# Kernel tuning notes

Hardware: AMD Instinct MI355X
Metric: run time of the kernel (lower is better)

The kernel has to match this reference:

```python
import jax, jax.numpy as jnp
import numpy as np

N_NODES = 50000
N_EDGES = 640000
D = 128
L = 3
LN_EPS = 1e-5


def _layer_norm(x, g, b):
    mu = jnp.mean(x, axis=-1, keepdims=True)
    var = jnp.mean(jnp.square(x - mu), axis=-1, keepdims=True)
    return (x - mu) * jax.lax.rsqrt(var + LN_EPS) * g + b


def setup_inputs() -> dict:
    key = jax.random.key(0)
    ks = jax.random.split(key, 8)
    scale = 1.0 / np.sqrt(D)
    x = jax.random.normal(ks[0], (N_NODES, D), dtype=jnp.float32)
    edge_index = jax.random.randint(ks[1], (2, N_EDGES), 0, N_NODES, dtype=jnp.int32)
    return {
        "x": x,
        "edge_index": edge_index,
        "eps": jnp.zeros((L,), jnp.float32),  # GIN epsilon, init 0.0
        "W1": jax.random.normal(ks[2], (L, D, D), jnp.float32) * scale,
        "b1": jnp.zeros((L, D), jnp.float32),
        "W2": jax.random.normal(ks[3], (L, D, D), jnp.float32) * scale,
        "b2": jnp.zeros((L, D), jnp.float32),
        "ln_g": jnp.ones((L, D), jnp.float32),   # per-conv LayerNorm
        "ln_b": jnp.zeros((L, D), jnp.float32),
        "skip_g": jnp.ones((L - 1, D), jnp.float32),  # outer norms for layers 0..L-2
        "skip_b": jnp.zeros((L - 1, D), jnp.float32),
    }


def reference(x, edge_index, eps, W1, b1, W2, b2, ln_g, ln_b, skip_g, skip_b):
    src = edge_index[0]
    dst = edge_index[1]
    h = x  # no input_norm (use_input_norm=False)
    for i in range(L):
        h_in = h
        # scatter-add neighbor aggregation: out[dst] += h[src]
        agg = jax.ops.segment_sum(h[src], dst, num_segments=N_NODES)
        z = (1.0 + eps[i]) * h + agg
        # 2-layer MLP: Linear -> ReLU -> Linear
        z = jnp.maximum(z @ W1[i] + b1[i], 0.0) @ W2[i] + b2[i]
        z = _layer_norm(z, ln_g[i], ln_b[i])
        if i < L - 1:
            z = _layer_norm(z, skip_g[i], skip_b[i])  # skip-path norm
            z = jnp.maximum(z, 0.0)  # ReLU; dropout is identity in eval
        h = z + h_in  # residual (shapes always match: in==hidden)
    return h
```

## Files before the change

### kernel.cpp

```cpp
#include <hip/hip_runtime.h>
#include <hip/hip_bf16.h>

#define N_NODES 50000
#define N_EDGES 640000
#define D 128
#define NPAD 50048
#define LAYERS 3
#define SCAN_NB 196

typedef __attribute__((ext_vector_type(4))) float f32x4;
typedef __attribute__((ext_vector_type(8))) short bf16x8;
typedef __attribute__((ext_vector_type(4))) short bf16x4;

static __device__ __forceinline__ short f2bf(float f) {
    union { float f; unsigned u; } x; x.f = f;
    unsigned r = x.u + 0x7fffu + ((x.u >> 16) & 1u);
    return (short)(r >> 16);
}
static __device__ __forceinline__ float bf2f(short s) {
    union { unsigned u; float f; } x; x.u = ((unsigned)(unsigned short)s) << 16;
    return x.f;
}

__global__ void init_kernel(const f32x4* __restrict__ in, bf16x4* __restrict__ hb) {
    int t = blockIdx.x * 256 + threadIdx.x;
    f32x4 v = in[t];
    bf16x4 p; p[0] = f2bf(v.x); p[1] = f2bf(v.y); p[2] = f2bf(v.z); p[3] = f2bf(v.w);
    hb[t] = p;
}

__global__ void prepw_kernel(const float* __restrict__ W1, const float* __restrict__ W2,
                             short* __restrict__ wt) {
    int t = blockIdx.x * 256 + threadIdx.x;
    if (t >= 6 * 16384) return;
    int m = t >> 14, rem = t & 16383;
    int c = rem >> 7, k = rem & 127;
    const float* src = (m < 3) ? (W1 + m * 16384) : (W2 + (m - 3) * 16384);
    wt[m * 16384 + c * 128 + k] = f2bf(src[k * 128 + c]);
}

__global__ void hist_kernel(const int* __restrict__ dst, int* __restrict__ deg) {
    int e = blockIdx.x * 256 + threadIdx.x;
    if (e < N_EDGES) atomicAdd(&deg[dst[e]], 1);
}

__global__ void scan1_kernel(const int* __restrict__ deg, int* __restrict__ rs,
                             int* __restrict__ bsum) {
    __shared__ int tmp[256];
    int i = blockIdx.x * 256 + threadIdx.x;
    int v = (i < N_NODES) ? deg[i] : 0;
    tmp[threadIdx.x] = v;
    __syncthreads();
    for (int off = 1; off < 256; off <<= 1) {
        int t = (threadIdx.x >= off) ? tmp[threadIdx.x - off] : 0;
        __syncthreads();
        tmp[threadIdx.x] += t;
        __syncthreads();
    }
    if (i < N_NODES) rs[i] = tmp[threadIdx.x] - v;
    if (threadIdx.x == 255) bsum[blockIdx.x] = tmp[255];
}

__global__ void scan2_kernel(int* __restrict__ bsum) {
    __shared__ int tmp[256];
    int v = (threadIdx.x < SCAN_NB) ? bsum[threadIdx.x] : 0;
    tmp[threadIdx.x] = v;
    __syncthreads();
    for (int off = 1; off < 256; off <<= 1) {
        int t = (threadIdx.x >= off) ? tmp[threadIdx.x - off] : 0;
        __syncthreads();
        tmp[threadIdx.x] += t;
        __syncthreads();
    }
    if (threadIdx.x < SCAN_NB) bsum[threadIdx.x] = tmp[threadIdx.x] - v;
}

__global__ void scan3_kernel(int* __restrict__ rs, const int* __restrict__ bsum) {
    int i = blockIdx.x * 256 + threadIdx.x;
    if (i < N_NODES) rs[i] += bsum[blockIdx.x];
}

__global__ void fill_kernel(const int* __restrict__ src, const int* __restrict__ dst,
                            const int* __restrict__ rs, int* __restrict__ cursor,
                            int* __restrict__ col) {
    int e = blockIdx.x * 256 + threadIdx.x;
    if (e >= N_EDGES) return;
    int d = dst[e];
    int p = atomicAdd(&cursor[d], 1);
    col[rs[d] + p] = src[e];
}

__global__ __launch_bounds__(256) void agg_kernel(const bf16x8* __restrict__ hb,
                                                  const int* __restrict__ rs,
                                                  const int* __restrict__ deg,
                                                  const int* __restrict__ col,
                                                  const float* __restrict__ epsArr, int layer,
                                                  bf16x8* __restrict__ z) {
    int t = blockIdx.x * 256 + threadIdx.x;
    int node = t >> 4, lane = t & 15;
    if (node >= NPAD) return;
    bf16x8 o;
    if (node < N_NODES) {
        float acc[8] = {0.f, 0.f, 0.f, 0.f, 0.f, 0.f, 0.f, 0.f};
        int start = rs[node], dg = deg[node];
        const int* cp = col + start;
        for (int base = 0; base < dg; base += 16) {
            int n = dg - base; n = n < 16 ? n : 16;
            int my = (lane < n) ? cp[base + lane] : 0;
            bf16x8 v[16];
#pragma unroll
            for (int j = 0; j < 16; ++j) {
                if (j < n) {
                    int idx = __shfl(my, j, 16);
                    v[j] = hb[(size_t)idx * 16 + lane];
                }
            }
#pragma unroll
            for (int j = 0; j < 16; ++j) {
                if (j < n) {
#pragma unroll
                    for (int e = 0; e < 8; ++e) acc[e] += bf2f(v[j][e]);
                }
            }
        }
        float s = 1.0f + epsArr[layer];
        bf16x8 hv = hb[(size_t)node * 16 + lane];
#pragma unroll
        for (int e = 0; e < 8; ++e) o[e] = f2bf(fmaf(s, bf2f(hv[e]), acc[e]));
    } else {
        o = (bf16x8)(short)0;
    }
    z[(size_t)node * 16 + lane] = o;
}

template <bool LAST>
__global__ __launch_bounds__(256, 2) void mlp_kernel(const short* __restrict__ Z,
                                                     const short* __restrict__ Wt1,
                                                     const float* __restrict__ B1,
                                                     const short* __restrict__ Wt2,
                                                     const float* __restrict__ B2,
                                                     const float* __restrict__ G1,
                                                     const float* __restrict__ Bt1,
                                                     const float* __restrict__ G2,
                                                     const float* __restrict__ Bt2,
                                                     const float* __restrict__ RS,
                                                     float* __restrict__ H,
                                                     short* __restrict__ HB) {
    __shared__ __align__(16) char lds[49152 + 3072];
    const int t = threadIdx.x;
    const int wave = t >> 6, lane = t & 63;
    const int r = lane & 15, kq = lane >> 4;
    const int lrow = wave * 16 + r;
    const int row = blockIdx.x * 64 + lrow;
    const int swzr = (r & 7) << 4;
    const int swzl = (lrow & 7) << 4;
    const int fcol = kq * 16;

    const short* Zr = Z + (size_t)row * D + kq * 8;
    bf16x8 zb0 = *(const bf16x8*)(Zr);
    bf16x8 zb1 = *(const bf16x8*)(Zr + 32);
    bf16x8 zb2 = *(const bf16x8*)(Zr + 64);
    bf16x8 zb3 = *(const bf16x8*)(Zr + 96);
    __builtin_amdgcn_sched_barrier(0);

    bf16x8 g2[8];
    {
        bf16x8 g1[8];
#pragma unroll
        for (int i = 0; i < 8; ++i) g1[i] = *(const bf16x8*)(Wt1 + i * 2048 + t * 8);
#pragma unroll
        for (int i = 0; i < 8; ++i) g2[i] = *(const bf16x8*)(Wt2 + i * 2048 + t * 8);
        if (t < (LAST ? 128 : 192)) {
            int which = t >> 5, chunk = t & 31;
            const float* vp = (which == 0) ? B1 : (which == 1) ? B2 : (which == 2) ? G1
                            : (which == 3) ? Bt1 : (which == 4) ? G2 : Bt2;
            *(f32x4*)(lds + 49152 + which * 512 + chunk * 16) = *(const f32x4*)(vp + chunk * 4);
        }
#pragma unroll
        for (int i = 0; i < 8; ++i) {
            int b = i * 4096 + t * 16;
            *(bf16x8*)(lds + (b ^ (((b >> 8) & 7) << 4))) = g1[i];
        }
    }
    __syncthreads();

    bf16x4 p[8];
#pragma unroll
    for (int ct = 0; ct < 8; ++ct) {
        int wb = (ct * 16 + r) * 256 + kq * 16;
        f32x4 acc = {0.f, 0.f, 0.f, 0.f};
        acc = __builtin_amdgcn_mfma_f32_16x16x32_bf16(*(const bf16x8*)(lds + ((wb      ) ^ swzr)), zb0, acc, 0, 0, 0);
        acc = __builtin_amdgcn_mfma_f32_16x16x32_bf16(*(const bf16x8*)(lds + ((wb +  64) ^ swzr)), zb1, acc, 0, 0, 0);
        acc = __builtin_amdgcn_mfma_f32_16x16x32_bf16(*(const bf16x8*)(lds + ((wb + 128) ^ swzr)), zb2, acc, 0, 0, 0);
        acc = __builtin_amdgcn_mfma_f32_16x16x32_bf16(*(const bf16x8*)(lds + ((wb + 192) ^ swzr)), zb3, acc, 0, 0, 0);
        f32x4 bias = *(const f32x4*)(lds + 49152 + 0 + ct * 64 + fcol);
        p[ct][0] = f2bf(fmaxf(acc[0] + bias.x, 0.0f));
        p[ct][1] = f2bf(fmaxf(acc[1] + bias.y, 0.0f));
        p[ct][2] = f2bf(fmaxf(acc[2] + bias.z, 0.0f));
        p[ct][3] = f2bf(fmaxf(acc[3] + bias.w, 0.0f));
    }
    __syncthreads();

    f32x4 rsv[8] = {};
    if (row < N_NODES) {
#pragma unroll
        for (int ct = 0; ct < 8; ++ct)
            rsv[ct] = *(const f32x4*)(RS + (size_t)row * D + ct * 16 + kq * 4);
    }
    __builtin_amdgcn_sched_barrier(0);

#pragma unroll
    for (int i = 0; i < 8; ++i) {
        int b = i * 4096 + t * 16;
        *(bf16x8*)(lds + (b ^ (((b >> 8) & 7) << 4))) = g2[i];
    }
#pragma unroll
    for (int ct = 0; ct < 8; ++ct)
        *(bf16x4*)(lds + 32768 + ((lrow * 256 + ct * 32 + kq * 8) ^ swzl)) = p[ct];
    __syncthreads();

    bf16x8 hb0 = *(const bf16x8*)(lds + 32768 + ((lrow * 256 +   0 + kq * 16) ^ swzl));
    bf16x8 hb1 = *(const bf16x8*)(lds + 32768 + ((lrow * 256 +  64 + kq * 16) ^ swzl));
    bf16x8 hb2 = *(const bf16x8*)(lds + 32768 + ((lrow * 256 + 128 + kq * 16) ^ swzl));
    bf16x8 hb3 = *(const bf16x8*)(lds + 32768 + ((lrow * 256 + 192 + kq * 16) ^ swzl));

    f32x4 o[8];
#pragma unroll
    for (int ct = 0; ct < 8; ++ct) {
        int wb = (ct * 16 + r) * 256 + kq * 16;
        f32x4 acc = {0.f, 0.f, 0.f, 0.f};
        acc = __builtin_amdgcn_mfma_f32_16x16x32_bf16(*(const bf16x8*)(lds + ((wb      ) ^ swzr)), hb0, acc, 0, 0, 0);
        acc = __builtin_amdgcn_mfma_f32_16x16x32_bf16(*(const bf16x8*)(lds + ((wb +  64) ^ swzr)), hb1, acc, 0, 0, 0);
        acc = __builtin_amdgcn_mfma_f32_16x16x32_bf16(*(const bf16x8*)(lds + ((wb + 128) ^ swzr)), hb2, acc, 0, 0, 0);
        acc = __builtin_amdgcn_mfma_f32_16x16x32_bf16(*(const bf16x8*)(lds + ((wb + 192) ^ swzr)), hb3, acc, 0, 0, 0);
        f32x4 bias = *(const f32x4*)(lds + 49152 + 512 + ct * 64 + fcol);
        o[ct] = acc + bias;
    }

    float s = 0.f, q = 0.f;
#pragma unroll
    for (int ct = 0; ct < 8; ++ct) {
        s += o[ct].x + o[ct].y + o[ct].z + o[ct].w;
        q += o[ct].x * o[ct].x + o[ct].y * o[ct].y + o[ct].z * o[ct].z + o[ct].w * o[ct].w;
    }
    s += __shfl_xor(s, 16, 64); q += __shfl_xor(q, 16, 64);
    s += __shfl_xor(s, 32, 64); q += __shfl_xor(q, 32, 64);
    float mu = s * (1.0f / D);
    float rstd = rsqrtf(q * (1.0f / D) - mu * mu + 1e-5f);
#pragma unroll
    for (int ct = 0; ct < 8; ++ct) {
        f32x4 g = *(const f32x4*)(lds + 49152 + 1024 + ct * 64 + fcol);
        f32x4 b = *(const f32x4*)(lds + 49152 + 1536 + ct * 64 + fcol);
        o[ct] = (o[ct] - mu) * rstd * g + b;
    }

    if (!LAST) {
        float s2 = 0.f, q2 = 0.f;
#pragma unroll
        for (int ct = 0; ct < 8; ++ct) {
            s2 += o[ct].x + o[ct].y + o[ct].z + o[ct].w;
            q2 += o[ct].x * o[ct].x + o[ct].y * o[ct].y + o[ct].z * o[ct].z + o[ct].w * o[ct].w;
        }
        s2 += __shfl_xor(s2, 16, 64); q2 += __shfl_xor(q2, 16, 64);
        s2 += __shfl_xor(s2, 32, 64); q2 += __shfl_xor(q2, 32, 64);
        float mu2 = s2 * (1.0f / D);
        float rstd2 = rsqrtf(q2 * (1.0f / D) - mu2 * mu2 + 1e-5f);
#pragma unroll
        for (int ct = 0; ct < 8; ++ct) {
            f32x4 g = *(const f32x4*)(lds + 49152 + 2048 + ct * 64 + fcol);
            f32x4 b = *(const f32x4*)(lds + 49152 + 2560 + ct * 64 + fcol);
            f32x4 y = (o[ct] - mu2) * rstd2 * g + b;
            y.x = fmaxf(y.x, 0.f); y.y = fmaxf(y.y, 0.f);
            y.z = fmaxf(y.z, 0.f); y.w = fmaxf(y.w, 0.f);
            o[ct] = y;
        }
    }

    if (row < N_NODES) {
#pragma unroll
        for (int ct = 0; ct < 8; ++ct) {
            size_t off = (size_t)row * D + ct * 16 + kq * 4;
            f32x4 hv = rsv[ct] + o[ct];
            *(f32x4*)(H + off) = hv;
            if (!LAST) {
                bf16x4 pb;
                pb[0] = f2bf(hv.x); pb[1] = f2bf(hv.y); pb[2] = f2bf(hv.z); pb[3] = f2bf(hv.w);
                *(bf16x4*)(HB + off) = pb;
            }
        }
    }
}

extern "C" void kernel_launch(void* const* d_in, const int* in_sizes, int n_in,
                              void* d_out, int out_size, void* d_ws, size_t ws_size,
                              hipStream_t stream) {
    const float* x   = (const float*)d_in[0];
    const int*   ei  = (const int*)d_in[1];
    const float* eps = (const float*)d_in[2];
    const float* W1  = (const float*)d_in[3];
    const float* b1  = (const float*)d_in[4];
    const float* W2  = (const float*)d_in[5];
    const float* b2  = (const float*)d_in[6];
    const float* lng = (const float*)d_in[7];
    const float* lnb = (const float*)d_in[8];
    const float* skg = (const float*)d_in[9];
    const float* skb = (const float*)d_in[10];
    float* h = (float*)d_out;

    char* ws = (char*)d_ws;
    short* zbuf = (short*)ws;
    short* hbb  = (short*)(ws + 12812288);
    short* wt   = (short*)(ws + 25624576);
    int*   rs   = (int*)  (ws + 25821184);
    int*   deg  = (int*)  (ws + 26021376);
    int*   cur  = (int*)  (ws + 26221568);
    int*   col  = (int*)  (ws + 26421760);
    int*   bsum = (int*)  (ws + 28981760);

    const int* srcIdx = ei;
    const int* dstIdx = ei + N_EDGES;

    init_kernel<<<(N_NODES * 32) / 256, 256, 0, stream>>>((const f32x4*)x, (bf16x4*)hbb);
    prepw_kernel<<<(6 * 16384) / 256, 256, 0, stream>>>(W1, W2, wt);

    hipMemsetAsync(deg, 0, 2 * 200192, stream);
    hist_kernel<<<(N_EDGES + 255) / 256, 256, 0, stream>>>(dstIdx, deg);
    scan1_kernel<<<SCAN_NB, 256, 0, stream>>>(deg, rs, bsum);
    scan2_kernel<<<1, 256, 0, stream>>>(bsum);
    scan3_kernel<<<SCAN_NB, 256, 0, stream>>>(rs, bsum);
    fill_kernel<<<(N_EDGES + 255) / 256, 256, 0, stream>>>(srcIdx, dstIdx, rs, cur, col);

    for (int l = 0; l < LAYERS; ++l) {
        agg_kernel<<<NPAD / 16, 256, 0, stream>>>(
            (const bf16x8*)hbb, rs, deg, col, eps, l, (bf16x8*)zbuf);
        const float* rsrc = (l == 0) ? x : h;
        if (l < LAYERS - 1) {
            mlp_kernel<false><<<NPAD / 64, 256, 0, stream>>>(
                zbuf, wt + l * 16384, b1 + l * D, wt + (3 + l) * 16384, b2 + l * D,
                lng + l * D, lnb + l * D, skg + l * D, skb + l * D, rsrc, h, hbb);
        } else {
            mlp_kernel<true><<<NPAD / 64, 256, 0, stream>>>(
                zbuf, wt + l * 16384, b1 + l * D, wt + (3 + l) * 16384, b2 + l * D,
                lng + l * D, lnb + l * D, nullptr, nullptr, rsrc, h, nullptr);
        }
    }
}
```

Measured before the change: 251.9 us.

## Fuse neighbor aggregation into MLP kernel with ping-pong bf16 feature buffers

Merges the separate gather/aggregation kernel into the MLP kernel. Each block now gathers neighbor rows for its 64 nodes with 4 threads per node and stages the aggregated z tile in LDS, instead of writing z to global memory and reading it back. The bf16 node features are double-buffered across layers so a layer reads one buffer while writing the other. This removes one launch per layer and the z round-trip through global memory. The cost is a gather with less parallelism: 4 lanes per node, each issuing 64-byte loads, versus the old 16 lanes with a shuffle-based index broadcast. It also puts more register pressure on a kernel launched with 2 blocks per SM.

Measured after the change: 235.7 us. -6.4%, faster.

```diff
diff --git a/kernel.cpp b/kernel.cpp
--- a/kernel.cpp
+++ b/kernel.cpp
@@ -90,62 +90,23 @@
     col[rs[d] + p] = src[e];
 }
 
-__global__ __launch_bounds__(256) void agg_kernel(const bf16x8* __restrict__ hb,
-                                                  const int* __restrict__ rs,
-                                                  const int* __restrict__ deg,
-                                                  const int* __restrict__ col,
-                                                  const float* __restrict__ epsArr, int layer,
-                                                  bf16x8* __restrict__ z) {
-    int t = blockIdx.x * 256 + threadIdx.x;
-    int node = t >> 4, lane = t & 15;
-    if (node >= NPAD) return;
-    bf16x8 o;
-    if (node < N_NODES) {
-        float acc[8] = {0.f, 0.f, 0.f, 0.f, 0.f, 0.f, 0.f, 0.f};
-        int start = rs[node], dg = deg[node];
-        const int* cp = col + start;
-        for (int base = 0; base < dg; base += 16) {
-            int n = dg - base; n = n < 16 ? n : 16;
-            int my = (lane < n) ? cp[base + lane] : 0;
-            bf16x8 v[16];
-#pragma unroll
-            for (int j = 0; j < 16; ++j) {
-                if (j < n) {
-                    int idx = __shfl(my, j, 16);
-                    v[j] = hb[(size_t)idx * 16 + lane];
-                }
-            }
-#pragma unroll
-            for (int j = 0; j < 16; ++j) {
-                if (j < n) {
-#pragma unroll
-                    for (int e = 0; e < 8; ++e) acc[e] += bf2f(v[j][e]);
-                }
-            }
-        }
-        float s = 1.0f + epsArr[layer];
-        bf16x8 hv = hb[(size_t)node * 16 + lane];
-#pragma unroll
-        for (int e = 0; e < 8; ++e) o[e] = f2bf(fmaf(s, bf2f(hv[e]), acc[e]));
-    } else {
-        o = (bf16x8)(short)0;
-    }
-    z[(size_t)node * 16 + lane] = o;
-}
-
 template <bool LAST>
-__global__ __launch_bounds__(256, 2) void mlp_kernel(const short* __restrict__ Z,
-                                                     const short* __restrict__ Wt1,
-                                                     const float* __restrict__ B1,
-                                                     const short* __restrict__ Wt2,
-                                                     const float* __restrict__ B2,
-                                                     const float* __restrict__ G1,
-                                                     const float* __restrict__ Bt1,
-                                                     const float* __restrict__ G2,
-                                                     const float* __restrict__ Bt2,
-                                                     const float* __restrict__ RS,
-                                                     float* __restrict__ H,
-                                                     short* __restrict__ HB) {
+__global__ __launch_bounds__(256, 2) void fused_kernel(const short* __restrict__ HBin,
+                                                       const int* __restrict__ rs,
+                                                       const int* __restrict__ deg,
+                                                       const int* __restrict__ col,
+                                                       const float* __restrict__ epsArr, int layer,
+                                                       const short* __restrict__ Wt1,
+                                                       const float* __restrict__ B1,
+                                                       const short* __restrict__ Wt2,
+                                                       const float* __restrict__ B2,
+                                                       const float* __restrict__ G1,
+                                                       const float* __restrict__ Bt1,
+                                                       const float* __restrict__ G2,
+                                                       const float* __restrict__ Bt2,
+                                                       const float* __restrict__ RS,
+                                                       float* __restrict__ H,
+                                                       short* __restrict__ HBout) {
     __shared__ __align__(16) char lds[49152 + 3072];
     const int t = threadIdx.x;
     const int wave = t >> 6, lane = t & 63;
@@ -155,59 +116,122 @@
     const int swzr = (r & 7) << 4;
     const int swzl = (lrow & 7) << 4;
     const int fcol = kq * 16;
-
-    const short* Zr = Z + (size_t)row * D + kq * 8;
-    bf16x8 zb0 = *(const bf16x8*)(Zr);
-    bf16x8 zb1 = *(const bf16x8*)(Zr + 32);
-    bf16x8 zb2 = *(const bf16x8*)(Zr + 64);
-    bf16x8 zb3 = *(const bf16x8*)(Zr + 96);
+    const int g = t >> 2, q = t & 3;
+    const int gnode = blockIdx.x * 64 + g;
+    const int gswz = (g & 7) << 4;
+
+    bf16x8 g1[8], g2[8];
+#pragma unroll
+    for (int i = 0; i < 8; ++i) g1[i] = *(const bf16x8*)(Wt1 + i * 2048 + t * 8);
+#pragma unroll
+    for (int i = 0; i < 8; ++i) g2[i] = *(const bf16x8*)(Wt2 + i * 2048 + t * 8);
     __builtin_amdgcn_sched_barrier(0);
 
-    bf16x8 g2[8];
-    {
-        bf16x8 g1[8];
-#pragma unroll
-        for (int i = 0; i < 8; ++i) g1[i] = *(const bf16x8*)(Wt1 + i * 2048 + t * 8);
-#pragma unroll
-        for (int i = 0; i < 8; ++i) g2[i] = *(const bf16x8*)(Wt2 + i * 2048 + t * 8);
-        if (t < (LAST ? 128 : 192)) {
-            int which = t >> 5, chunk = t & 31;
-            const float* vp = (which == 0) ? B1 : (which == 1) ? B2 : (which == 2) ? G1
-                            : (which == 3) ? Bt1 : (which == 4) ? G2 : Bt2;
-            *(f32x4*)(lds + 49152 + which * 512 + chunk * 16) = *(const f32x4*)(vp + chunk * 4);
-        }
-#pragma unroll
-        for (int i = 0; i < 8; ++i) {
-            int b = i * 4096 + t * 16;
-            *(bf16x8*)(lds + (b ^ (((b >> 8) & 7) << 4))) = g1[i];
-        }
-    }
-    __syncthreads();
+    float acc[32];
+#pragma unroll
+    for (int i = 0; i < 32; ++i) acc[i] = 0.f;
+    if (gnode < N_NODES) {
+        int start = rs[gnode], dg = deg[gnode];
+        const int* cp = col + start;
+        const short* tab = HBin + q * 32;
+        int e = 0;
+        for (; e + 2 <= dg; e += 2) {
+            const short* r0 = tab + (size_t)cp[e] * 128;
+            const short* r1 = tab + (size_t)cp[e + 1] * 128;
+            bf16x8 a0 = *(const bf16x8*)(r0);
+            bf16x8 a1 = *(const bf16x8*)(r0 + 8);
+            bf16x8 a2 = *(const bf16x8*)(r0 + 16);
+            bf16x8 a3 = *(const bf16x8*)(r0 + 24);
+            bf16x8 b0 = *(const bf16x8*)(r1);
+            bf16x8 b1 = *(const bf16x8*)(r1 + 8);
+            bf16x8 b2 = *(const bf16x8*)(r1 + 16);
+            bf16x8 b3 = *(const bf16x8*)(r1 + 24);
+#pragma unroll
+            for (int j = 0; j < 8; ++j) {
+                acc[j]      += bf2f(a0[j]) + bf2f(b0[j]);
+                acc[8 + j]  += bf2f(a1[j]) + bf2f(b1[j]);
+                acc[16 + j] += bf2f(a2[j]) + bf2f(b2[j]);
+                acc[24 + j] += bf2f(a3[j]) + bf2f(b3[j]);
+            }
+        }
+        if (e < dg) {
+            const short* r0 = tab + (size_t)cp[e] * 128;
+            bf16x8 a0 = *(const bf16x8*)(r0);
+            bf16x8 a1 = *(const bf16x8*)(r0 + 8);
+            bf16x8 a2 = *(const bf16x8*)(r0 + 16);
+            bf16x8 a3 = *(const bf16x8*)(r0 + 24);
+#pragma unroll
+            for (int j = 0; j < 8; ++j) {
+                acc[j]      += bf2f(a0[j]);
+                acc[8 + j]  += bf2f(a1[j]);
+                acc[16 + j] += bf2f(a2[j]);
+                acc[24 + j] += bf2f(a3[j]);
+            }
+        }
+        float s = 1.0f + epsArr[layer];
+        const short* hs = tab + (size_t)gnode * 128;
+        bf16x8 h0 = *(const bf16x8*)(hs);
+        bf16x8 h1 = *(const bf16x8*)(hs + 8);
+        bf16x8 h2 = *(const bf16x8*)(hs + 16);
+        bf16x8 h3 = *(const bf16x8*)(hs + 24);
+#pragma unroll
+        for (int j = 0; j < 8; ++j) {
+            acc[j]      = fmaf(s, bf2f(h0[j]), acc[j]);
+            acc[8 + j]  = fmaf(s, bf2f(h1[j]), acc[8 + j]);
+            acc[16 + j] = fmaf(s, bf2f(h2[j]), acc[16 + j]);
+            acc[24 + j] = fmaf(s, bf2f(h3[j]), acc[24 + j]);
+        }
+    }
+    bf16x8 zp[4];
+#pragma unroll
+    for (int i = 0; i < 4; ++i) {
+#pragma unroll
+        for (int j = 0; j < 8; ++j) zp[i][j] = f2bf(acc[i * 8 + j]);
+    }
+
+    if (t < (LAST ? 128 : 192)) {
+        int which = t >> 5, chunk = t & 31;
+        const float* vp = (which == 0) ? B1 : (which == 1) ? B2 : (which == 2) ? G1
+                        : (which == 3) ? Bt1 : (which == 4) ? G2 : Bt2;
+        *(f32x4*)(lds + 49152 + which * 512 + chunk * 16) = *(const f32x4*)(vp + chunk * 4);
+    }
+#pragma unroll
+    for (int i = 0; i < 8; ++i) {
+        int b = i * 4096 + t * 16;
+        *(bf16x8*)(lds + (b ^ (((b >> 8) & 7) << 4))) = g1[i];
+    }
+#pragma unroll
+    for (int i = 0; i < 4; ++i)
+        *(bf16x8*)(lds + 32768 + ((g * 256 + q * 64 + i * 16) ^ gswz)) = zp[i];
+    __syncthreads();
+
+    bf16x8 zb0 = *(const bf16x8*)(lds + 32768 + ((lrow * 256 +   0 + kq * 16) ^ swzl));
+    bf16x8 zb1 = *(const bf16x8*)(lds + 32768 + ((lrow * 256 +  64 + kq * 16) ^ swzl));
+    bf16x8 zb2 = *(const bf16x8*)(lds + 32768 + ((lrow * 256 + 128 + kq * 16) ^ swzl));
+    bf16x8 zb3 = *(const bf16x8*)(lds + 32768 + ((lrow * 256 + 192 + kq * 16) ^ swzl));
+    f32x4 rsv[8] = {};
+    if (row < N_NODES) {
+#pragma unroll
+        for (int ct = 0; ct < 8; ++ct)
+            rsv[ct] = *(const f32x4*)(RS + (size_t)row * D + ct * 16 + kq * 4);
+    }
 
     bf16x4 p[8];
 #pragma unroll
     for (int ct = 0; ct < 8; ++ct) {
         int wb = (ct * 16 + r) * 256 + kq * 16;
-        f32x4 acc = {0.f, 0.f, 0.f, 0.f};
-        acc = __builtin_amdgcn_mfma_f32_16x16x32_bf16(*(const bf16x8*)(lds + ((wb      ) ^ swzr)), zb0, acc, 0, 0, 0);
-        acc = __builtin_amdgcn_mfma_f32_16x16x32_bf16(*(const bf16x8*)(lds + ((wb +  64) ^ swzr)), zb1, acc, 0, 0, 0);
-        acc = __builtin_amdgcn_mfma_f32_16x16x32_bf16(*(const bf16x8*)(lds + ((wb + 128) ^ swzr)), zb2, acc, 0, 0, 0);
-        acc = __builtin_amdgcn_mfma_f32_16x16x32_bf16(*(const bf16x8*)(lds + ((wb + 192) ^ swzr)), zb3, acc, 0, 0, 0);
+        f32x4 a = {0.f, 0.f, 0.f, 0.f};
+        a = __builtin_amdgcn_mfma_f32_16x16x32_bf16(*(const bf16x8*)(lds + ((wb      ) ^ swzr)), zb0, a, 0, 0, 0);
+        a = __builtin_amdgcn_mfma_f32_16x16x32_bf16(*(const bf16x8*)(lds + ((wb +  64) ^ swzr)), zb1, a, 0, 0, 0);
+        a = __builtin_amdgcn_mfma_f32_16x16x32_bf16(*(const bf16x8*)(lds + ((wb + 128) ^ swzr)), zb2, a, 0, 0, 0);
+        a = __builtin_amdgcn_mfma_f32_16x16x32_bf16(*(const bf16x8*)(lds + ((wb + 192) ^ swzr)), zb3, a, 0, 0, 0);
         f32x4 bias = *(const f32x4*)(lds + 49152 + 0 + ct * 64 + fcol);
-        p[ct][0] = f2bf(fmaxf(acc[0] + bias.x, 0.0f));
-        p[ct][1] = f2bf(fmaxf(acc[1] + bias.y, 0.0f));
-        p[ct][2] = f2bf(fmaxf(acc[2] + bias.z, 0.0f));
-        p[ct][3] = f2bf(fmaxf(acc[3] + bias.w, 0.0f));
-    }
-    __syncthreads();
-
-    f32x4 rsv[8] = {};
-    if (row < N_NODES) {
-#pragma unroll
-        for (int ct = 0; ct < 8; ++ct)
-            rsv[ct] = *(const f32x4*)(RS + (size_t)row * D + ct * 16 + kq * 4);
-    }
-    __builtin_amdgcn_sched_barrier(0);
+        p[ct][0] = f2bf(fmaxf(a[0] + bias.x, 0.0f));
+        p[ct][1] = f2bf(fmaxf(a[1] + bias.y, 0.0f));
+        p[ct][2] = f2bf(fmaxf(a[2] + bias.z, 0.0f));
+        p[ct][3] = f2bf(fmaxf(a[3] + bias.w, 0.0f));
+    }
+    __syncthreads();
 
 #pragma unroll
     for (int i = 0; i < 8; ++i) {
@@ -228,30 +252,30 @@
 #pragma unroll
     for (int ct = 0; ct < 8; ++ct) {
         int wb = (ct * 16 + r) * 256 + kq * 16;
-        f32x4 acc = {0.f, 0.f, 0.f, 0.f};
-        acc = __builtin_amdgcn_mfma_f32_16x16x32_bf16(*(const bf16x8*)(lds + ((wb      ) ^ swzr)), hb0, acc, 0, 0, 0);
-        acc = __builtin_amdgcn_mfma_f32_16x16x32_bf16(*(const bf16x8*)(lds + ((wb +  64) ^ swzr)), hb1, acc, 0, 0, 0);
-        acc = __builtin_amdgcn_mfma_f32_16x16x32_bf16(*(const bf16x8*)(lds + ((wb + 128) ^ swzr)), hb2, acc, 0, 0, 0);
-        acc = __builtin_amdgcn_mfma_f32_16x16x32_bf16(*(const bf16x8*)(lds + ((wb + 192) ^ swzr)), hb3, acc, 0, 0, 0);
+        f32x4 a = {0.f, 0.f, 0.f, 0.f};
+        a = __builtin_amdgcn_mfma_f32_16x16x32_bf16(*(const bf16x8*)(lds + ((wb      ) ^ swzr)), hb0, a, 0, 0, 0);
+        a = __builtin_amdgcn_mfma_f32_16x16x32_bf16(*(const bf16x8*)(lds + ((wb +  64) ^ swzr)), hb1, a, 0, 0, 0);
+        a = __builtin_amdgcn_mfma_f32_16x16x32_bf16(*(const bf16x8*)(lds + ((wb + 128) ^ swzr)), hb2, a, 0, 0, 0);
+        a = __builtin_amdgcn_mfma_f32_16x16x32_bf16(*(const bf16x8*)(lds + ((wb + 192) ^ swzr)), hb3, a, 0, 0, 0);
         f32x4 bias = *(const f32x4*)(lds + 49152 + 512 + ct * 64 + fcol);
-        o[ct] = acc + bias;
-    }
-
-    float s = 0.f, q = 0.f;
+        o[ct] = a + bias;
+    }
+
+    float s = 0.f, qq = 0.f;
 #pragma unroll
     for (int ct = 0; ct < 8; ++ct) {
-        s += o[ct].x + o[ct].y + o[ct].z + o[ct].w;
-        q += o[ct].x * o[ct].x + o[ct].y * o[ct].y + o[ct].z * o[ct].z + o[ct].w * o[ct].w;
-    }
-    s += __shfl_xor(s, 16, 64); q += __shfl_xor(q, 16, 64);
-    s += __shfl_xor(s, 32, 64); q += __shfl_xor(q, 32, 64);
+        s  += o[ct].x + o[ct].y + o[ct].z + o[ct].w;
+        qq += o[ct].x * o[ct].x + o[ct].y * o[ct].y + o[ct].z * o[ct].z + o[ct].w * o[ct].w;
+    }
+    s += __shfl_xor(s, 16, 64); qq += __shfl_xor(qq, 16, 64);
+    s += __shfl_xor(s, 32, 64); qq += __shfl_xor(qq, 32, 64);
     float mu = s * (1.0f / D);
-    float rstd = rsqrtf(q * (1.0f / D) - mu * mu + 1e-5f);
+    float rstd = rsqrtf(qq * (1.0f / D) - mu * mu + 1e-5f);
 #pragma unroll
     for (int ct = 0; ct < 8; ++ct) {
-        f32x4 g = *(const f32x4*)(lds + 49152 + 1024 + ct * 64 + fcol);
-        f32x4 b = *(const f32x4*)(lds + 49152 + 1536 + ct * 64 + fcol);
-        o[ct] = (o[ct] - mu) * rstd * g + b;
+        f32x4 gv = *(const f32x4*)(lds + 49152 + 1024 + ct * 64 + fcol);
+        f32x4 bv = *(const f32x4*)(lds + 49152 + 1536 + ct * 64 + fcol);
+        o[ct] = (o[ct] - mu) * rstd * gv + bv;
     }
 
     if (!LAST) {
@@ -267,9 +291,9 @@
         float rstd2 = rsqrtf(q2 * (1.0f / D) - mu2 * mu2 + 1e-5f);
 #pragma unroll
         for (int ct = 0; ct < 8; ++ct) {
-            f32x4 g = *(const f32x4*)(lds + 49152 + 2048 + ct * 64 + fcol);
-            f32x4 b = *(const f32x4*)(lds + 49152 + 2560 + ct * 64 + fcol);
-            f32x4 y = (o[ct] - mu2) * rstd2 * g + b;
+            f32x4 gv = *(const f32x4*)(lds + 49152 + 2048 + ct * 64 + fcol);
+            f32x4 bv = *(const f32x4*)(lds + 49152 + 2560 + ct * 64 + fcol);
+            f32x4 y = (o[ct] - mu2) * rstd2 * gv + bv;
             y.x = fmaxf(y.x, 0.f); y.y = fmaxf(y.y, 0.f);
             y.z = fmaxf(y.z, 0.f); y.w = fmaxf(y.w, 0.f);
             o[ct] = y;
@@ -285,7 +309,7 @@
             if (!LAST) {
                 bf16x4 pb;
                 pb[0] = f2bf(hv.x); pb[1] = f2bf(hv.y); pb[2] = f2bf(hv.z); pb[3] = f2bf(hv.w);
-                *(bf16x4*)(HB + off) = pb;
+                *(bf16x4*)(HBout + off) = pb;
             }
         }
     }
@@ -308,19 +332,19 @@
     float* h = (float*)d_out;
 
     char* ws = (char*)d_ws;
-    short* zbuf = (short*)ws;
-    short* hbb  = (short*)(ws + 12812288);
-    short* wt   = (short*)(ws + 25624576);
-    int*   rs   = (int*)  (ws + 25821184);
-    int*   deg  = (int*)  (ws + 26021376);
-    int*   cur  = (int*)  (ws + 26221568);
-    int*   col  = (int*)  (ws + 26421760);
-    int*   bsum = (int*)  (ws + 28981760);
+    short* hb0  = (short*)ws;
+    short* hb1  = (short*)(ws + 12800000);
+    short* wt   = (short*)(ws + 25600000);
+    int*   rs   = (int*)  (ws + 25796608);
+    int*   deg  = (int*)  (ws + 25996800);
+    int*   cur  = (int*)  (ws + 26196992);
+    int*   col  = (int*)  (ws + 26397184);
+    int*   bsum = (int*)  (ws + 28957184);
 
     const int* srcIdx = ei;
     const int* dstIdx = ei + N_EDGES;
 
-    init_kernel<<<(N_NODES * 32) / 256, 256, 0, stream>>>((const f32x4*)x, (bf16x4*)hbb);
+    init_kernel<<<(N_NODES * 32) / 256, 256, 0, stream>>>((const f32x4*)x, (bf16x4*)hb0);
     prepw_kernel<<<(6 * 16384) / 256, 256, 0, stream>>>(W1, W2, wt);
 
     hipMemsetAsync(deg, 0, 2 * 200192, stream);
@@ -330,17 +354,20 @@
     scan3_kernel<<<SCAN_NB, 256, 0, stream>>>(rs, bsum);
     fill_kernel<<<(N_EDGES + 255) / 256, 256, 0, stream>>>(srcIdx, dstIdx, rs, cur, col);
 
+    short* hbs[2] = {hb0, hb1};
     for (int l = 0; l < LAYERS; ++l) {
-        agg_kernel<<<NPAD / 16, 256, 0, stream>>>(
-            (const bf16x8*)hbb, rs, deg, col, eps, l, (bf16x8*)zbuf);
         const float* rsrc = (l == 0) ? x : h;
+        short* hin  = hbs[l & 1];
+        short* hout = hbs[(l + 1) & 1];
         if (l < LAYERS - 1) {
-            mlp_kernel<false><<<NPAD / 64, 256, 0, stream>>>(
-                zbuf, wt + l * 16384, b1 + l * D, wt + (3 + l) * 16384, b2 + l * D,
-                lng + l * D, lnb + l * D, skg + l * D, skb + l * D, rsrc, h, hbb);
+            fused_kernel<false><<<NPAD / 64, 256, 0, stream>>>(
+                hin, rs, deg, col, eps, l,
+                wt + l * 16384, b1 + l * D, wt + (3 + l) * 16384, b2 + l * D,
+                lng + l * D, lnb + l * D, skg + l * D, skb + l * D, rsrc, h, hout);
         } else {
-            mlp_kernel<true><<<NPAD / 64, 256, 0, stream>>>(
-                zbuf, wt + l * 16384, b1 + l * D, wt + (3 + l) * 16384, b2 + l * D,
+            fused_kernel<true><<<NPAD / 64, 256, 0, stream>>>(
+                hin, rs, deg, col, eps, l,
+                wt + l * 16384, b1 + l * D, wt + (3 + l) * 16384, b2 + l * D,
                 lng + l * D, lnb + l * D, nullptr, nullptr, rsrc, h, nullptr);
         }
     }
```

## Rewrite neighbor aggregation to stage gathered rows into LDS via global_load_lds

Applied to the files above, without the earlier changes.

The aggregation kernel now assigns one wave per node, processed sequentially over 16 nodes per wave. Each wave issues up to 32 direct global-to-LDS 4-byte loads per neighbor chunk into a per-wave ring buffer, then each lane accumulates two bf16 features from LDS. The aim is to raise memory-level parallelism and cut register pressure compared with the previous 16-lanes-per-node register gather. In exchange, each lane loads only 4 bytes per row, so transactions are narrower. Column indices are read as uniform scalar loads and nodes within a wave run serially, so latency may be exposed.

After: 460.4 us. 1.83x slower.

```diff
diff --git a/kernel.cpp b/kernel.cpp
--- a/kernel.cpp
+++ b/kernel.cpp
@@ -17,9 +17,13 @@
     unsigned r = x.u + 0x7fffu + ((x.u >> 16) & 1u);
     return (short)(r >> 16);
 }
-static __device__ __forceinline__ float bf2f(short s) {
-    union { unsigned u; float f; } x; x.u = ((unsigned)(unsigned short)s) << 16;
-    return x.f;
+static __device__ __forceinline__ float ubits(unsigned u) {
+    union { unsigned u; float f; } x; x.u = u; return x.f;
+}
+
+static __device__ __forceinline__ void gload4(const void* g, void* l) {
+    __builtin_amdgcn_global_load_lds((const __attribute__((address_space(1))) unsigned*)g,
+                                     (__attribute__((address_space(3))) unsigned*)l, 4, 0, 0);
 }
 
 __global__ void init_kernel(const f32x4* __restrict__ in, bf16x4* __restrict__ hb) {
@@ -90,47 +94,54 @@
     col[rs[d] + p] = src[e];
 }
 
-__global__ __launch_bounds__(256) void agg_kernel(const bf16x8* __restrict__ hb,
+__global__ __launch_bounds__(256) void agg_kernel(const short* __restrict__ hb,
                                                   const int* __restrict__ rs,
                                                   const int* __restrict__ deg,
                                                   const int* __restrict__ col,
                                                   const float* __restrict__ epsArr, int layer,
-                                                  bf16x8* __restrict__ z) {
-    int t = blockIdx.x * 256 + threadIdx.x;
-    int node = t >> 4, lane = t & 15;
-    if (node >= NPAD) return;
-    bf16x8 o;
-    if (node < N_NODES) {
-        float acc[8] = {0.f, 0.f, 0.f, 0.f, 0.f, 0.f, 0.f, 0.f};
-        int start = rs[node], dg = deg[node];
-        const int* cp = col + start;
-        for (int base = 0; base < dg; base += 16) {
-            int n = dg - base; n = n < 16 ? n : 16;
-            int my = (lane < n) ? cp[base + lane] : 0;
-            bf16x8 v[16];
-#pragma unroll
-            for (int j = 0; j < 16; ++j) {
-                if (j < n) {
-                    int idx = __shfl(my, j, 16);
-                    v[j] = hb[(size_t)idx * 16 + lane];
+                                                  unsigned* __restrict__ z) {
+    __shared__ __align__(16) char ring[4][32][256];
+    const int wave = threadIdx.x >> 6, lane = threadIdx.x & 63;
+    const char* hbase = (const char*)hb;
+    char* myring = &ring[wave][0][0];
+    const float s = 1.0f + epsArr[layer];
+
+    for (int i = 0; i < 16; ++i) {
+        int node = blockIdx.x * 64 + wave * 16 + i;
+        float accx = 0.f, accy = 0.f;
+        if (node < N_NODES) {
+            int start = rs[node], d = deg[node];
+            const int* cp = col + start;
+            for (int c0 = 0; c0 < d; c0 += 32) {
+                int n = d - c0; n = n < 32 ? n : 32;
+                asm volatile("s_waitcnt lgkmcnt(0)" ::: "memory");
+                __builtin_amdgcn_sched_barrier(0);
+#pragma unroll
+                for (int j = 0; j < 32; ++j) {
+                    if (j < n) {
+                        int idx = cp[c0 + j];
+                        gload4(hbase + ((size_t)idx << 8) + (lane << 2), myring + j * 256);
+                    }
+                }
+                asm volatile("s_waitcnt vmcnt(0)" ::: "memory");
+                __builtin_amdgcn_sched_barrier(0);
+#pragma unroll
+                for (int j = 0; j < 32; ++j) {
+                    if (j < n) {
+                        unsigned u = *(const unsigned*)(myring + j * 256 + (lane << 2));
+                        accx += ubits(u << 16);
+                        accy += ubits(u & 0xFFFF0000u);
+                    }
                 }
             }
-#pragma unroll
-            for (int j = 0; j < 16; ++j) {
-                if (j < n) {
-#pragma unroll
-                    for (int e = 0; e < 8; ++e) acc[e] += bf2f(v[j][e]);
-                }
-            }
-        }
-        float s = 1.0f + epsArr[layer];
-        bf16x8 hv = hb[(size_t)node * 16 + lane];
-#pragma unroll
-        for (int e = 0; e < 8; ++e) o[e] = f2bf(fmaf(s, bf2f(hv[e]), acc[e]));
-    } else {
-        o = (bf16x8)(short)0;
-    }
-    z[(size_t)node * 16 + lane] = o;
+            unsigned su = *(const unsigned*)(hbase + ((size_t)node << 8) + (lane << 2));
+            accx = fmaf(s, ubits(su << 16), accx);
+            accy = fmaf(s, ubits(su & 0xFFFF0000u), accy);
+        }
+        unsigned out = (unsigned)(unsigned short)f2bf(accx)
+                     | ((unsigned)(unsigned short)f2bf(accy) << 16);
+        z[(size_t)node * 64 + lane] = out;
+    }
 }
 
 template <bool LAST>
@@ -331,8 +342,8 @@
     fill_kernel<<<(N_EDGES + 255) / 256, 256, 0, stream>>>(srcIdx, dstIdx, rs, cur, col);
 
     for (int l = 0; l < LAYERS; ++l) {
-        agg_kernel<<<NPAD / 16, 256, 0, stream>>>(
-            (const bf16x8*)hbb, rs, deg, col, eps, l, (bf16x8*)zbuf);
+        agg_kernel<<<NPAD / 64, 256, 0, stream>>>(
+            hbb, rs, deg, col, eps, l, (unsigned*)zbuf);
         const float* rsrc = (l == 0) ? x : h;
         if (l < LAYERS - 1) {
             mlp_kernel<false><<<NPAD / 64, 256, 0, stream>>>(
```
